# Kernel tuning notes

Measured on AMD Instinct MI355X. Metric: run time of the kernel, lower is better.

The kernel has to match this reference:

```python
import jax, jax.numpy as jnp
import numpy as np

B, NP, N, C, H = 16, 512, 1024, 1024, 16
HD = C // H
HID = 4 * C
EPS = 1e-5


def _layernorm(x, g, b):
    mu = jnp.mean(x, axis=-1, keepdims=True)
    var = jnp.mean(jnp.square(x - mu), axis=-1, keepdims=True)
    return (x - mu) * jax.lax.rsqrt(var + EPS) * g + b


def setup_inputs() -> dict:
    key = jax.random.key(0)
    ks = jax.random.split(key, 12)
    x = jax.random.normal(ks[0], (B, NP, C), dtype=jnp.float32)
    cache_k = jax.random.normal(ks[1], (B, H, N, HD), dtype=jnp.float32)
    cache_v = jax.random.normal(ks[2], (B, H, N, HD), dtype=jnp.float32)
    # update_mask: exactly NP active (to-be-updated) token slots per batch row
    scores = jax.random.uniform(ks[3], (B, N))
    top = jnp.argsort(scores, axis=1)[:, :NP]
    update_mask = jnp.zeros((B, N), dtype=bool).at[jnp.arange(B)[:, None], top].set(True)
    s = 0.02
    qkv_w = jax.random.normal(ks[4], (C, 3 * C), dtype=jnp.float32) * s
    qkv_b = jnp.zeros((3 * C,), dtype=jnp.float32)
    proj_w = jax.random.normal(ks[5], (C, C), dtype=jnp.float32) * s
    proj_b = jnp.zeros((C,), dtype=jnp.float32)
    n1_g = jnp.ones((C,), dtype=jnp.float32)
    n1_b = jnp.zeros((C,), dtype=jnp.float32)
    n2_g = jnp.ones((C,), dtype=jnp.float32)
    n2_b = jnp.zeros((C,), dtype=jnp.float32)
    fc1_w = jax.random.normal(ks[6], (C, HID), dtype=jnp.float32) * s
    fc1_b = jnp.zeros((HID,), dtype=jnp.float32)
    fc2_w = jax.random.normal(ks[7], (HID, C), dtype=jnp.float32) * s
    fc2_b = jnp.zeros((C,), dtype=jnp.float32)
    return dict(x=x, cache_k=cache_k, cache_v=cache_v, update_mask=update_mask,
                qkv_w=qkv_w, qkv_b=qkv_b, proj_w=proj_w, proj_b=proj_b,
                n1_g=n1_g, n1_b=n1_b, n2_g=n2_g, n2_b=n2_b,
                fc1_w=fc1_w, fc1_b=fc1_b, fc2_w=fc2_w, fc2_b=fc2_b)


def reference(x, cache_k, cache_v, update_mask, qkv_w, qkv_b, proj_w, proj_b,
              n1_g, n1_b, n2_g, n2_b, fc1_w, fc1_b, fc2_w, fc2_b):
    Bq, Np, Cd = x.shape
    h = _layernorm(x, n1_g, n1_b)
    qkv = (h @ qkv_w + qkv_b).reshape(Bq, Np, 3, H, HD)
    q, k, v = jnp.moveaxis(qkv, 2, 0)               # each [B, Np, H, HD]
    q = jnp.swapaxes(q, 1, 2)                       # [B, H, Np, HD]
    k = jnp.swapaxes(k, 1, 2)
    v = jnp.swapaxes(v, 1, 2)
    # masked_scatter_: i-th new token -> i-th masked slot (row-uniform mask count)
    idx = jnp.argsort(jnp.logical_not(update_mask), axis=1)[:, :Np]  # [B, Np]
    k_full = jax.vmap(lambda c, i, kn: c.at[:, i, :].set(kn))(cache_k, idx, k)
    v_full = jax.vmap(lambda c, i, vn: c.at[:, i, :].set(vn))(cache_v, idx, v)
    scale = HD ** -0.5
    attn = jnp.einsum('bhqd,bhkd->bhqk', q * scale, k_full)  # [B,H,Np,N]
    attn = jax.nn.softmax(attn, axis=-1)
    o = jnp.einsum('bhqk,bhkd->bhqd', attn, v_full)
    o = jnp.swapaxes(o, 1, 2).reshape(Bq, Np, Cd)
    o = o @ proj_w + proj_b
    x = x + o
    h2 = _layernorm(x, n2_g, n2_b)
    mlp = jax.nn.gelu(h2 @ fc1_w + fc1_b, approximate=False) @ fc2_w + fc2_b
    return x + mlp
```

## Files before the change

kernel.cpp:

```cpp
#include <hip/hip_runtime.h>
#include <hip/hip_bf16.h>
#include <math.h>

#define Bd   16
#define NPd  512
#define Nd   1024
#define Cd   1024
#define Hd   16
#define HDd  64
#define HIDd 4096
#define EPSd 1e-5f
#define MRd  (Bd * NPd)

typedef unsigned short u16;
typedef __bf16 bf16x8 __attribute__((ext_vector_type(8)));
typedef float  f32x4  __attribute__((ext_vector_type(4)));

__device__ __forceinline__ u16 f2bf(float f) {
    unsigned int u = __builtin_bit_cast(unsigned int, f);
    u = u + 0x7fffu + ((u >> 16) & 1u);
    return (u16)(u >> 16);
}

__device__ __forceinline__ void async_load16(const void* g, void* l) {
    __builtin_amdgcn_global_load_lds(
        (const __attribute__((address_space(1))) void*)(uintptr_t)g,
        (__attribute__((address_space(3))) void*)(unsigned int)(uintptr_t)l,
        16, 0, 0);
}

__global__ __launch_bounds__(256) void build_src(const void* __restrict__ mask_raw,
                                                 int* __restrict__ src) {
    const int b = blockIdx.x;
    const int t = threadIdx.x;
    const unsigned char* m8 = (const unsigned char*)mask_raw;
    const int* m32 = (const int*)mask_raw;

    int c = 0;
    #pragma unroll
    for (int i = 0; i < 4; i++) c += (m8[b * Nd + t * 4 + i] != 0) ? 1 : 0;
    #pragma unroll
    for (int off = 1; off < 64; off <<= 1) c += __shfl_xor(c, off);
    __shared__ int warr[4];
    if ((t & 63) == 0) warr[t >> 6] = c;
    __syncthreads();
    const int c8 = warr[0] + warr[1] + warr[2] + warr[3];
    const bool use8 = (c8 == NPd);

    int f[4];
    #pragma unroll
    for (int i = 0; i < 4; i++) {
        const int n = t * 4 + i;
        f[i] = use8 ? (m8[b * Nd + n] != 0) : (m32[b * Nd + n] != 0);
    }
    const int loc = f[0] + f[1] + f[2] + f[3];

    int sc_ = loc;
    #pragma unroll
    for (int off = 1; off < 64; off <<= 1) {
        const int u = __shfl_up(sc_, off);
        if ((t & 63) >= off) sc_ += u;
    }
    __shared__ int wtot[4];
    __syncthreads();
    if ((t & 63) == 63) wtot[t >> 6] = sc_;
    __syncthreads();
    int base = 0;
    for (int w = 0; w < (t >> 6); w++) base += wtot[w];

    int run = base + sc_ - loc;
    #pragma unroll
    for (int i = 0; i < 4; i++) {
        const int n = t * 4 + i;
        src[b * Nd + n] = f[i] ? run : -1;
        run += f[i];
    }
}

__global__ __launch_bounds__(256) void ln_kernel(const float* __restrict__ x,
                                                 const float* __restrict__ g,
                                                 const float* __restrict__ bb,
                                                 u16* __restrict__ out) {
    const int row = blockIdx.x;
    const int t = threadIdx.x;
    const float* xr = x + (size_t)row * Cd;
    const float4 v = *(const float4*)(xr + t * 4);
    float s = v.x + v.y + v.z + v.w;
    float q = v.x * v.x + v.y * v.y + v.z * v.z + v.w * v.w;
    #pragma unroll
    for (int off = 1; off < 64; off <<= 1) {
        s += __shfl_xor(s, off);
        q += __shfl_xor(q, off);
    }
    __shared__ float ss[4], qq[4];
    if ((t & 63) == 0) { ss[t >> 6] = s; qq[t >> 6] = q; }
    __syncthreads();
    s = ss[0] + ss[1] + ss[2] + ss[3];
    q = qq[0] + qq[1] + qq[2] + qq[3];
    const float mu = s * (1.0f / Cd);
    const float var = q * (1.0f / Cd) - mu * mu;
    const float rs = rsqrtf(var + EPSd);
    const float4 gv = *(const float4*)(g + t * 4);
    const float4 bv = *(const float4*)(bb + t * 4);
    ushort4 r;
    r.x = f2bf((v.x - mu) * rs * gv.x + bv.x);
    r.y = f2bf((v.y - mu) * rs * gv.y + bv.y);
    r.z = f2bf((v.z - mu) * rs * gv.z + bv.z);
    r.w = f2bf((v.w - mu) * rs * gv.w + bv.w);
    *(ushort4*)(out + (size_t)row * Cd + t * 4) = r;
}

__global__ __launch_bounds__(256) void conv_t(const float* __restrict__ W,
                                              u16* __restrict__ Wt,
                                              int K, int N) {
    __shared__ float tile[32][33];
    const int k0 = blockIdx.y * 32;
    const int n0 = blockIdx.x * 32;
    const int t = threadIdx.x;
    const int row = t >> 3, c4 = (t & 7) * 4;
    const float4 v = *(const float4*)(W + (size_t)(k0 + row) * N + n0 + c4);
    tile[row][c4 + 0] = v.x;
    tile[row][c4 + 1] = v.y;
    tile[row][c4 + 2] = v.z;
    tile[row][c4 + 3] = v.w;
    __syncthreads();
    ushort4 o;
    o.x = f2bf(tile[c4 + 0][row]);
    o.y = f2bf(tile[c4 + 1][row]);
    o.z = f2bf(tile[c4 + 2][row]);
    o.w = f2bf(tile[c4 + 3][row]);
    *(ushort4*)(Wt + (size_t)(n0 + row) * K + k0 + c4) = o;
}

template <int EPI, typename OUT_T>
__global__ __launch_bounds__(256) void gemm_mfma(const u16* __restrict__ A,
                                                 const u16* __restrict__ Wt,
                                                 const float* __restrict__ bias,
                                                 const float* __restrict__ res,
                                                 OUT_T* __restrict__ out,
                                                 int K, int Nn) {
    __shared__ u16 As[3][128 * 32];
    __shared__ u16 Bs[3][128 * 32];

    const int t = threadIdx.x;
    const int L = t & 63;
    const int w = t >> 6;
    const int wm = w >> 1, wn = w & 1;

    const int gx = gridDim.x;
    const int nwg = gx * gridDim.y;
    int id = blockIdx.y * gx + blockIdx.x;
    id = (id & 7) * (nwg >> 3) + (id >> 3);
    const int m0 = (id / gx) * 128;
    const int n0 = (id % gx) * 128;

    const int srow = 32 * w + (L >> 2);
    const int scol = (((L & 3) ^ ((L >> 3) & 3)) * 8);
    const u16* ap0 = A  + (size_t)(m0 + srow) * K + scol;
    const u16* ap1 = ap0 + (size_t)16 * K;
    const u16* bp0 = Wt + (size_t)(n0 + srow) * K + scol;
    const u16* bp1 = bp0 + (size_t)16 * K;

    f32x4 acc[4][4];
    const f32x4 zero = {0.f, 0.f, 0.f, 0.f};
    #pragma unroll
    for (int i = 0; i < 4; i++)
        #pragma unroll
        for (int j = 0; j < 4; j++) acc[i][j] = zero;

    const int rr = L & 15;
    const int frag_off = rr * 32 + ((((L >> 4)) ^ ((rr >> 1) & 3)) * 8);
    const int nsteps = K >> 5;

#define STAGE_G(s_, kt_) do {                                   \
        const int off_ = (kt_) << 5;                            \
        async_load16(ap0 + off_, &As[s_][w * 1024]);            \
        async_load16(ap1 + off_, &As[s_][w * 1024 + 512]);      \
        async_load16(bp0 + off_, &Bs[s_][w * 1024]);            \
        async_load16(bp1 + off_, &Bs[s_][w * 1024 + 512]);      \
    } while (0)

    STAGE_G(0, 0);
    STAGE_G(1, 1);
    asm volatile("s_waitcnt vmcnt(4)" ::: "memory");
    __builtin_amdgcn_s_barrier();

    int cur = 0;
    for (int kt = 0; kt < nsteps; kt++) {
        if (kt + 2 < nsteps) {
            int s2 = cur + 2; if (s2 >= 3) s2 -= 3;
            STAGE_G(s2, kt + 2);
        }

        bf16x8 a[4], b[4];
        #pragma unroll
        for (int i = 0; i < 4; i++) {
            a[i] = *(const bf16x8*)&As[cur][(wm * 64 + i * 16) * 32 + frag_off];
            b[i] = *(const bf16x8*)&Bs[cur][(wn * 64 + i * 16) * 32 + frag_off];
        }
        #pragma unroll
        for (int i = 0; i < 4; i++)
            #pragma unroll
            for (int j = 0; j < 4; j++)
                acc[i][j] = __builtin_amdgcn_mfma_f32_16x16x32_bf16(a[i], b[j], acc[i][j], 0, 0, 0);

        if (kt + 2 < nsteps) asm volatile("s_waitcnt vmcnt(4)" ::: "memory");
        else                 asm volatile("s_waitcnt vmcnt(0)" ::: "memory");
        __builtin_amdgcn_s_barrier();
        cur = (cur + 1 == 3) ? 0 : cur + 1;
    }
#undef STAGE_G

    const int cn = n0 + wn * 64 + (L & 15);
    const int cm = m0 + wm * 64 + (L >> 4) * 4;
    #pragma unroll
    for (int i = 0; i < 4; i++) {
        #pragma unroll
        for (int j = 0; j < 4; j++) {
            const int nn = cn + j * 16;
            const float bv = bias[nn];
            #pragma unroll
            for (int r = 0; r < 4; r++) {
                const int mm = cm + i * 16 + r;
                float v = acc[i][j][r] + bv;
                if (EPI == 2) v = 0.5f * v * (1.0f + erff(v * 0.70710678118654752f));
                if (EPI == 1) v += res[(size_t)mm * Nn + nn];
                if constexpr (sizeof(OUT_T) == 2) out[(size_t)mm * Nn + nn] = (OUT_T)f2bf(v);
                else out[(size_t)mm * Nn + nn] = v;
            }
        }
    }
}

__global__ __launch_bounds__(256) void kv_cast(const u16* __restrict__ qkv,
                                               const float* __restrict__ ck,
                                               const float* __restrict__ cv,
                                               const int* __restrict__ srcArr,
                                               u16* __restrict__ Kb,
                                               u16* __restrict__ Vtb) {
    const int id = blockIdx.x;
    const int nt = id & 15, hh = (id >> 4) & 15, b = id >> 8;
    const int t = threadIdx.x;
    __shared__ u16 Vl[64][72];

    const int row = t >> 2;
    const int dd = (t & 3) * 16;
    const int n = nt * 64 + row;
    const int sidx = srcArr[b * Nd + n];

    u16 kv16[16], vv16[16];
    if (sidx >= 0) {
        const u16* kp = qkv + (size_t)(b * NPd + sidx) * 3072 + Cd + hh * 64 + dd;
        const u16* vp = kp + Cd;
        *(ulonglong2*)&kv16[0] = *(const ulonglong2*)kp;
        *(ulonglong2*)&kv16[8] = *(const ulonglong2*)(kp + 8);
        *(ulonglong2*)&vv16[0] = *(const ulonglong2*)vp;
        *(ulonglong2*)&vv16[8] = *(const ulonglong2*)(vp + 8);
    } else {
        const float* kp = ck + ((size_t)((b * Hd + hh) * Nd + n)) * HDd + dd;
        const float* vp = cv + ((size_t)((b * Hd + hh) * Nd + n)) * HDd + dd;
        #pragma unroll
        for (int c = 0; c < 4; c++) {
            const float4 kc4 = *(const float4*)(kp + c * 4);
            const float4 vc4 = *(const float4*)(vp + c * 4);
            kv16[c * 4 + 0] = f2bf(kc4.x); kv16[c * 4 + 1] = f2bf(kc4.y);
            kv16[c * 4 + 2] = f2bf(kc4.z); kv16[c * 4 + 3] = f2bf(kc4.w);
            vv16[c * 4 + 0] = f2bf(vc4.x); vv16[c * 4 + 1] = f2bf(vc4.y);
            vv16[c * 4 + 2] = f2bf(vc4.z); vv16[c * 4 + 3] = f2bf(vc4.w);
        }
    }

    u16* ko = Kb + ((size_t)((b * Hd + hh) * Nd + n)) * HDd + dd;
    *(ulonglong2*)ko = *(ulonglong2*)&kv16[0];
    *(ulonglong2*)(ko + 8) = *(ulonglong2*)&kv16[8];

    #pragma unroll
    for (int i = 0; i < 16; i++) Vl[row][dd + i] = vv16[i];
    __syncthreads();

    const int d = t >> 2, nc = (t & 3) * 16;
    u16 ov[16];
    #pragma unroll
    for (int i = 0; i < 16; i++) ov[i] = Vl[nc + i][d];
    u16* vo = Vtb + ((size_t)((b * Hd + hh) * HDd + d)) * Nd + nt * 64 + nc;
    *(ulonglong2*)vo = *(ulonglong2*)&ov[0];
    *(ulonglong2*)(vo + 8) = *(ulonglong2*)&ov[8];
}

__global__ __launch_bounds__(256) void attn_mfma(const u16* __restrict__ qkv,
                                                 const u16* __restrict__ Kb,
                                                 const u16* __restrict__ Vtb,
                                                 u16* __restrict__ attno) {
    const int orig = blockIdx.y * 256 + blockIdx.x;
    const int xc = orig & 7, pos = orig >> 3;
    const int bh = (xc << 5) | (pos >> 3);
    const int qt = pos & 7;
    const int b = bh >> 4, hh = bh & 15;
    const int t = threadIdx.x;
    const int L = t & 63;
    const int w = t >> 6;

    __shared__ u16 Qs[4096];
    __shared__ u16 Ks[4096];
    __shared__ u16 Vs[4096];
    __shared__ u16 Ps[4][16 * 72];

    const size_t kbase = (size_t)((b * Hd + hh) * Nd) * HDd;
    const size_t vbase = (size_t)((b * Hd + hh) * HDd) * Nd;

    #pragma unroll
    for (int j = 0; j < 2; j++) {
        const int row = 16 * w + 8 * j + (L >> 3);
        const int ch = (L & 7) ^ (row & 7);
        const u16* g = qkv + (size_t)(b * NPd + qt * 64 + row) * 3072 + hh * 64 + ch * 8;
        async_load16(g, Qs + (16 * w + 8 * j) * 64);
    }

    f32x4 acc[4];
    const f32x4 zero = {0.f, 0.f, 0.f, 0.f};
    #pragma unroll
    for (int nb = 0; nb < 4; nb++) acc[nb] = zero;
    float m_run[4] = {-INFINITY, -INFINITY, -INFINITY, -INFINITY};
    float l_run[4] = {0.f, 0.f, 0.f, 0.f};

    for (int kt = 0; kt < 16; kt++) {
        __syncthreads();
        #pragma unroll
        for (int j = 0; j < 2; j++) {
            const int row = 16 * w + 8 * j + (L >> 3);
            const int ch = (L & 7) ^ (row & 7);
            async_load16(Kb + kbase + (size_t)(kt * 64 + row) * 64 + ch * 8,
                         Ks + (16 * w + 8 * j) * 64);
            async_load16(Vtb + vbase + (size_t)row * Nd + kt * 64 + ch * 8,
                         Vs + (16 * w + 8 * j) * 64);
        }
        __syncthreads();

        const int qrow = 16 * w + (L & 15);
        const bf16x8 aq0 = *(const bf16x8*)&Qs[qrow * 64 + (((L >> 4)     ^ (L & 7)) * 8)];
        const bf16x8 aq1 = *(const bf16x8*)&Qs[qrow * 64 + (((4 + (L >> 4)) ^ (L & 7)) * 8)];

        f32x4 s[4];
        #pragma unroll
        for (int kb = 0; kb < 4; kb++) {
            const int krow = kb * 16 + (L & 15);
            const bf16x8 bk0 = *(const bf16x8*)&Ks[krow * 64 + (((L >> 4)     ^ (L & 7)) * 8)];
            const bf16x8 bk1 = *(const bf16x8*)&Ks[krow * 64 + (((4 + (L >> 4)) ^ (L & 7)) * 8)];
            s[kb] = __builtin_amdgcn_mfma_f32_16x16x32_bf16(aq0, bk0, zero, 0, 0, 0);
            s[kb] = __builtin_amdgcn_mfma_f32_16x16x32_bf16(aq1, bk1, s[kb], 0, 0, 0);
        }

        float al[4];
        float pb[4][4];
        #pragma unroll
        for (int r = 0; r < 4; r++) {
            float m = fmaxf(fmaxf(s[0][r], s[1][r]), fmaxf(s[2][r], s[3][r])) * 0.125f;
            m = fmaxf(m, __shfl_xor(m, 1));
            m = fmaxf(m, __shfl_xor(m, 2));
            m = fmaxf(m, __shfl_xor(m, 4));
            m = fmaxf(m, __shfl_xor(m, 8));
            const float mn = fmaxf(m_run[r], m);
            al[r] = __expf(m_run[r] - mn);
            m_run[r] = mn;
        }
        float ps[4] = {0.f, 0.f, 0.f, 0.f};
        #pragma unroll
        for (int kb = 0; kb < 4; kb++)
            #pragma unroll
            for (int r = 0; r < 4; r++) {
                const float p = __expf(s[kb][r] * 0.125f - m_run[r]);
                pb[kb][r] = p;
                ps[r] += p;
            }
        #pragma unroll
        for (int r = 0; r < 4; r++) {
            ps[r] += __shfl_xor(ps[r], 1);
            ps[r] += __shfl_xor(ps[r], 2);
            ps[r] += __shfl_xor(ps[r], 4);
            ps[r] += __shfl_xor(ps[r], 8);
            l_run[r] = l_run[r] * al[r] + ps[r];
        }
        #pragma unroll
        for (int nb = 0; nb < 4; nb++)
            #pragma unroll
            for (int r = 0; r < 4; r++) acc[nb][r] *= al[r];

        u16* pw = &Ps[w][0];
        #pragma unroll
        for (int kb = 0; kb < 4; kb++)
            #pragma unroll
            for (int r = 0; r < 4; r++)
                pw[((L >> 4) * 4 + r) * 72 + kb * 16 + (L & 15)] = f2bf(pb[kb][r]);

        const bf16x8 ap0 = *(const bf16x8*)&Ps[w][(L & 15) * 72 +      (L >> 4) * 8];
        const bf16x8 ap1 = *(const bf16x8*)&Ps[w][(L & 15) * 72 + 32 + (L >> 4) * 8];
        #pragma unroll
        for (int nb = 0; nb < 4; nb++) {
            const int drow = nb * 16 + (L & 15);
            const bf16x8 bv0 = *(const bf16x8*)&Vs[drow * 64 + (((L >> 4)     ^ (L & 7)) * 8)];
            const bf16x8 bv1 = *(const bf16x8*)&Vs[drow * 64 + (((4 + (L >> 4)) ^ (L & 7)) * 8)];
            acc[nb] = __builtin_amdgcn_mfma_f32_16x16x32_bf16(ap0, bv0, acc[nb], 0, 0, 0);
            acc[nb] = __builtin_amdgcn_mfma_f32_16x16x32_bf16(ap1, bv1, acc[nb], 0, 0, 0);
        }
    }

    float inv[4];
    #pragma unroll
    for (int r = 0; r < 4; r++) inv[r] = 1.0f / l_run[r];
    #pragma unroll
    for (int nb = 0; nb < 4; nb++)
        #pragma unroll
        for (int r = 0; r < 4; r++) {
            const int q = qt * 64 + w * 16 + (L >> 4) * 4 + r;
            const int d = nb * 16 + (L & 15);
            attno[(size_t)(b * NPd + q) * Cd + hh * 64 + d] = f2bf(acc[nb][r] * inv[r]);
        }
}

extern "C" void kernel_launch(void* const* d_in, const int* in_sizes, int n_in,
                              void* d_out, int out_size, void* d_ws, size_t ws_size,
                              hipStream_t stream) {
    const float* x       = (const float*)d_in[0];
    const float* cache_k = (const float*)d_in[1];
    const float* cache_v = (const float*)d_in[2];
    const void*  mask    = d_in[3];
    const float* qkv_w   = (const float*)d_in[4];
    const float* qkv_b   = (const float*)d_in[5];
    const float* proj_w  = (const float*)d_in[6];
    const float* proj_b  = (const float*)d_in[7];
    const float* n1_g    = (const float*)d_in[8];
    const float* n1_b    = (const float*)d_in[9];
    const float* n2_g    = (const float*)d_in[10];
    const float* n2_b    = (const float*)d_in[11];
    const float* fc1_w   = (const float*)d_in[12];
    const float* fc1_b   = (const float*)d_in[13];
    const float* fc2_w   = (const float*)d_in[14];
    const float* fc2_b   = (const float*)d_in[15];
    float* out = (float*)d_out;

    const size_t MR = (size_t)Bd * NPd;
    char* ws = (char*)d_ws;
    int*   srcArr = (int*)ws;
    float* x2     = (float*)(ws + 65536);
    u16*   h      = (u16*)(x2 + MR * Cd);
    u16*   attno  = h + MR * Cd;
    u16*   qkv    = attno + MR * Cd;
    u16*   Kb     = qkv + MR * 3 * Cd;
    u16*   Vtb    = Kb + (size_t)Bd * Hd * Nd * HDd;
    u16*   m1     = qkv;
    u16*   qkv_wt = Vtb + (size_t)Bd * Hd * Nd * HDd;
    u16*   proj_wt= qkv_wt + (size_t)3 * Cd * Cd;
    u16*   fc1_wt = proj_wt + (size_t)Cd * Cd;
    u16*   fc2_wt = fc1_wt + (size_t)Cd * HIDd;

    build_src<<<Bd, 256, 0, stream>>>(mask, srcArr);
    conv_t<<<dim3(3 * Cd / 32, Cd / 32),  256, 0, stream>>>(qkv_w,  qkv_wt,  Cd,   3 * Cd);
    conv_t<<<dim3(Cd / 32, Cd / 32),      256, 0, stream>>>(proj_w, proj_wt, Cd,   Cd);
    conv_t<<<dim3(HIDd / 32, Cd / 32),    256, 0, stream>>>(fc1_w,  fc1_wt,  Cd,   HIDd);
    conv_t<<<dim3(Cd / 32, HIDd / 32),    256, 0, stream>>>(fc2_w,  fc2_wt,  HIDd, Cd);

    ln_kernel<<<MR, 256, 0, stream>>>(x, n1_g, n1_b, h);
    gemm_mfma<0, u16><<<dim3(3 * Cd / 128, MR / 128), 256, 0, stream>>>(
        h, qkv_wt, qkv_b, nullptr, qkv, Cd, 3 * Cd);
    kv_cast<<<Bd * Hd * (Nd / 64), 256, 0, stream>>>(qkv, cache_k, cache_v, srcArr, Kb, Vtb);
    attn_mfma<<<dim3(Bd * Hd, NPd / 64), 256, 0, stream>>>(qkv, Kb, Vtb, attno);
    gemm_mfma<1, float><<<dim3(Cd / 128, MR / 128), 256, 0, stream>>>(
        attno, proj_wt, proj_b, x, x2, Cd, Cd);
    ln_kernel<<<MR, 256, 0, stream>>>(x2, n2_g, n2_b, h);
    gemm_mfma<2, u16><<<dim3(HIDd / 128, MR / 128), 256, 0, stream>>>(
        h, fc1_wt, fc1_b, nullptr, m1, Cd, HIDd);
    gemm_mfma<1, float><<<dim3(Cd / 128, MR / 128), 256, 0, stream>>>(
        m1, fc2_wt, fc2_b, x2, out, HIDd, Cd);
}
```

Measured before the change: 637.2 us.

## Transpose QK MFMA, lazy softmax rescale, and keep Q fragments in registers

Swaps the operands of the QK^T MFMA so each lane holds one query's scores. Row max and sum then need only two cross-lane shuffles, and the running max/sum become scalars. The softmax rescale is skipped unless some max grows by more than a threshold of 8 (lazy rescaling), P is written to LDS as packed 4-element stores, and Q fragments are loaded from LDS once instead of every tile. It adds shuffles to redistribute the alpha and 1/l factors into the PV accumulator layout, and it relies on a bounded exponent growth assumption for numerical safety.

```diff
diff --git a/kernel.cpp b/kernel.cpp
--- a/kernel.cpp
+++ b/kernel.cpp
@@ -299,6 +299,8 @@
     const int t = threadIdx.x;
     const int L = t & 63;
     const int w = t >> 6;
+    const int g = L >> 4;
+    const int q16 = L & 15;
 
     __shared__ u16 Qs[4096];
     __shared__ u16 Ks[4096];
@@ -312,16 +314,18 @@
     for (int j = 0; j < 2; j++) {
         const int row = 16 * w + 8 * j + (L >> 3);
         const int ch = (L & 7) ^ (row & 7);
-        const u16* g = qkv + (size_t)(b * NPd + qt * 64 + row) * 3072 + hh * 64 + ch * 8;
-        async_load16(g, Qs + (16 * w + 8 * j) * 64);
+        const u16* gq = qkv + (size_t)(b * NPd + qt * 64 + row) * 3072 + hh * 64 + ch * 8;
+        async_load16(gq, Qs + (16 * w + 8 * j) * 64);
     }
 
     f32x4 acc[4];
     const f32x4 zero = {0.f, 0.f, 0.f, 0.f};
     #pragma unroll
     for (int nb = 0; nb < 4; nb++) acc[nb] = zero;
-    float m_run[4] = {-INFINITY, -INFINITY, -INFINITY, -INFINITY};
-    float l_run[4] = {0.f, 0.f, 0.f, 0.f};
+    float m_run = -INFINITY;
+    float l_run = 0.f;
+
+    bf16x8 aq0, aq1;
 
     for (int kt = 0; kt < 16; kt++) {
         __syncthreads();
@@ -336,83 +340,83 @@
         }
         __syncthreads();
 
-        const int qrow = 16 * w + (L & 15);
-        const bf16x8 aq0 = *(const bf16x8*)&Qs[qrow * 64 + (((L >> 4)     ^ (L & 7)) * 8)];
-        const bf16x8 aq1 = *(const bf16x8*)&Qs[qrow * 64 + (((4 + (L >> 4)) ^ (L & 7)) * 8)];
+        if (kt == 0) {
+            const int qrow = 16 * w + q16;
+            aq0 = *(const bf16x8*)&Qs[qrow * 64 + ((g       ^ (L & 7)) * 8)];
+            aq1 = *(const bf16x8*)&Qs[qrow * 64 + (((4 + g) ^ (L & 7)) * 8)];
+        }
 
         f32x4 s[4];
         #pragma unroll
         for (int kb = 0; kb < 4; kb++) {
-            const int krow = kb * 16 + (L & 15);
-            const bf16x8 bk0 = *(const bf16x8*)&Ks[krow * 64 + (((L >> 4)     ^ (L & 7)) * 8)];
-            const bf16x8 bk1 = *(const bf16x8*)&Ks[krow * 64 + (((4 + (L >> 4)) ^ (L & 7)) * 8)];
-            s[kb] = __builtin_amdgcn_mfma_f32_16x16x32_bf16(aq0, bk0, zero, 0, 0, 0);
-            s[kb] = __builtin_amdgcn_mfma_f32_16x16x32_bf16(aq1, bk1, s[kb], 0, 0, 0);
-        }
-
-        float al[4];
-        float pb[4][4];
-        #pragma unroll
-        for (int r = 0; r < 4; r++) {
-            float m = fmaxf(fmaxf(s[0][r], s[1][r]), fmaxf(s[2][r], s[3][r])) * 0.125f;
-            m = fmaxf(m, __shfl_xor(m, 1));
-            m = fmaxf(m, __shfl_xor(m, 2));
-            m = fmaxf(m, __shfl_xor(m, 4));
-            m = fmaxf(m, __shfl_xor(m, 8));
-            const float mn = fmaxf(m_run[r], m);
-            al[r] = __expf(m_run[r] - mn);
-            m_run[r] = mn;
-        }
-        float ps[4] = {0.f, 0.f, 0.f, 0.f};
-        #pragma unroll
-        for (int kb = 0; kb < 4; kb++)
+            const int krow = kb * 16 + q16;
+            const bf16x8 bk0 = *(const bf16x8*)&Ks[krow * 64 + ((g       ^ (L & 7)) * 8)];
+            const bf16x8 bk1 = *(const bf16x8*)&Ks[krow * 64 + (((4 + g) ^ (L & 7)) * 8)];
+            s[kb] = __builtin_amdgcn_mfma_f32_16x16x32_bf16(bk0, aq0, zero, 0, 0, 0);
+            s[kb] = __builtin_amdgcn_mfma_f32_16x16x32_bf16(bk1, aq1, s[kb], 0, 0, 0);
+        }
+
+        float m0 = fmaxf(fmaxf(s[0][0], s[0][1]), fmaxf(s[0][2], s[0][3]));
+        float m1 = fmaxf(fmaxf(s[1][0], s[1][1]), fmaxf(s[1][2], s[1][3]));
+        float m2 = fmaxf(fmaxf(s[2][0], s[2][1]), fmaxf(s[2][2], s[2][3]));
+        float m3 = fmaxf(fmaxf(s[3][0], s[3][1]), fmaxf(s[3][2], s[3][3]));
+        float mx = fmaxf(fmaxf(m0, m1), fmaxf(m2, m3)) * 0.125f;
+        mx = fmaxf(mx, __shfl_xor(mx, 16));
+        mx = fmaxf(mx, __shfl_xor(mx, 32));
+
+        if (__any(mx > m_run + 8.f)) {
+            const float mn = fmaxf(m_run, mx);
+            const float al = __expf(m_run - mn);
+            m_run = mn;
+            l_run *= al;
+            float alr[4];
             #pragma unroll
-            for (int r = 0; r < 4; r++) {
-                const float p = __expf(s[kb][r] * 0.125f - m_run[r]);
-                pb[kb][r] = p;
-                ps[r] += p;
-            }
-        #pragma unroll
-        for (int r = 0; r < 4; r++) {
-            ps[r] += __shfl_xor(ps[r], 1);
-            ps[r] += __shfl_xor(ps[r], 2);
-            ps[r] += __shfl_xor(ps[r], 4);
-            ps[r] += __shfl_xor(ps[r], 8);
-            l_run[r] = l_run[r] * al[r] + ps[r];
-        }
-        #pragma unroll
-        for (int nb = 0; nb < 4; nb++)
+            for (int r = 0; r < 4; r++) alr[r] = __shfl(al, g * 4 + r);
             #pragma unroll
-            for (int r = 0; r < 4; r++) acc[nb][r] *= al[r];
+            for (int nb = 0; nb < 4; nb++)
+                #pragma unroll
+                for (int r = 0; r < 4; r++) acc[nb][r] *= alr[r];
+        }
 
         u16* pw = &Ps[w][0];
-        #pragma unroll
-        for (int kb = 0; kb < 4; kb++)
-            #pragma unroll
-            for (int r = 0; r < 4; r++)
-                pw[((L >> 4) * 4 + r) * 72 + kb * 16 + (L & 15)] = f2bf(pb[kb][r]);
-
-        const bf16x8 ap0 = *(const bf16x8*)&Ps[w][(L & 15) * 72 +      (L >> 4) * 8];
-        const bf16x8 ap1 = *(const bf16x8*)&Ps[w][(L & 15) * 72 + 32 + (L >> 4) * 8];
+        float ps = 0.f;
+        #pragma unroll
+        for (int kb = 0; kb < 4; kb++) {
+            float p0 = __expf(fmaf(s[kb][0], 0.125f, -m_run));
+            float p1 = __expf(fmaf(s[kb][1], 0.125f, -m_run));
+            float p2 = __expf(fmaf(s[kb][2], 0.125f, -m_run));
+            float p3 = __expf(fmaf(s[kb][3], 0.125f, -m_run));
+            ps += (p0 + p1) + (p2 + p3);
+            ushort4 v4;
+            v4.x = f2bf(p0); v4.y = f2bf(p1); v4.z = f2bf(p2); v4.w = f2bf(p3);
+            *(ushort4*)&pw[q16 * 72 + kb * 16 + g * 4] = v4;
+        }
+        ps += __shfl_xor(ps, 16);
+        ps += __shfl_xor(ps, 32);
+        l_run += ps;
+
+        const bf16x8 ap0 = *(const bf16x8*)&Ps[w][q16 * 72 +      g * 8];
+        const bf16x8 ap1 = *(const bf16x8*)&Ps[w][q16 * 72 + 32 + g * 8];
         #pragma unroll
         for (int nb = 0; nb < 4; nb++) {
-            const int drow = nb * 16 + (L & 15);
-            const bf16x8 bv0 = *(const bf16x8*)&Vs[drow * 64 + (((L >> 4)     ^ (L & 7)) * 8)];
-            const bf16x8 bv1 = *(const bf16x8*)&Vs[drow * 64 + (((4 + (L >> 4)) ^ (L & 7)) * 8)];
+            const int drow = nb * 16 + q16;
+            const bf16x8 bv0 = *(const bf16x8*)&Vs[drow * 64 + ((g       ^ (L & 7)) * 8)];
+            const bf16x8 bv1 = *(const bf16x8*)&Vs[drow * 64 + (((4 + g) ^ (L & 7)) * 8)];
             acc[nb] = __builtin_amdgcn_mfma_f32_16x16x32_bf16(ap0, bv0, acc[nb], 0, 0, 0);
             acc[nb] = __builtin_amdgcn_mfma_f32_16x16x32_bf16(ap1, bv1, acc[nb], 0, 0, 0);
         }
     }
 
+    const float invq = 1.0f / l_run;
     float inv[4];
     #pragma unroll
-    for (int r = 0; r < 4; r++) inv[r] = 1.0f / l_run[r];
+    for (int r = 0; r < 4; r++) inv[r] = __shfl(invq, g * 4 + r);
     #pragma unroll
     for (int nb = 0; nb < 4; nb++)
         #pragma unroll
         for (int r = 0; r < 4; r++) {
-            const int q = qt * 64 + w * 16 + (L >> 4) * 4 + r;
-            const int d = nb * 16 + (L & 15);
+            const int q = qt * 64 + w * 16 + g * 4 + r;
+            const int d = nb * 16 + q16;
             attno[(size_t)(b * NPd + q) * Cd + hh * 64 + d] = f2bf(acc[nb][r] * inv[r]);
         }
 }
```

Measured after the change: 607.0 us. 1.05x faster.
